# Kernel optimization log

Hardware: AMD Instinct MI355X
Metric: run time of the kernel (lower is better)

The kernel has to match this reference:

```python
import jax, jax.numpy as jnp
import numpy as np
import math

NUM_CLASSES = 80
IMG = 800
LEVELS = [3, 4, 5, 6, 7]
LOW_T, HIGH_T = 0.4, 0.5  # Matcher thresholds


def _make_anchors():
    """detectron2 DefaultAnchorGenerator: sizes 2^(i+2)*2^(k/3), ratios {0.5,1,2}, offset 0.5."""
    all_anchors = []
    for i in LEVELS:
        stride = 2 ** i
        fs = math.ceil(IMG / stride)
        sizes = [2 ** (i + 2) * 2 ** (k / 3.0) for k in range(3)]
        cell = []
        for s in sizes:  # sizes outer, ratios inner (detectron2 order)
            area = s * s
            for a in (0.5, 1.0, 2.0):
                w = math.sqrt(area / a)
                h = a * w
                cell.append([-w / 2.0, -h / 2.0, w / 2.0, h / 2.0])
        cell = np.asarray(cell, np.float32)  # [9, 4]
        coords = (np.arange(fs, dtype=np.float32) + 0.5) * stride
        sx, sy = np.meshgrid(coords, coords)  # row-major (y, x)
        shifts = np.stack([sx.ravel(), sy.ravel(), sx.ravel(), sy.ravel()], axis=1)
        all_anchors.append((shifts[:, None, :] + cell[None, :, :]).reshape(-1, 4))
    return np.concatenate(all_anchors, 0)  # [120087, 4] xyxy


def setup_inputs() -> dict:
    key = jax.random.key(0)
    k1, k2, k3 = jax.random.split(key, 3)
    anchors = jnp.asarray(_make_anchors())  # [A, 4]
    B, T = 8, 64
    cxy = jax.random.uniform(k1, (B, T, 2), jnp.float32, 0.0, float(IMG))
    wh = jax.random.uniform(k2, (B, T, 2), jnp.float32, 10.0, 300.0)
    tgt_boxes = jnp.concatenate([cxy, wh], axis=-1)  # [B, T, 4] cxcywh
    tgt_labels = jax.random.randint(k3, (B, T), 0, NUM_CLASSES, jnp.int32)
    return {"anchors": anchors, "tgt_boxes": tgt_boxes, "tgt_labels": tgt_labels}


def _cxcywh_to_xyxy(b):
    cx, cy, w, h = b[..., 0], b[..., 1], b[..., 2], b[..., 3]
    return jnp.stack([cx - 0.5 * w, cy - 0.5 * h, cx + 0.5 * w, cy + 0.5 * h], axis=-1)


def _pairwise_iou(a, b):
    # a: [T,4], b: [A,4] xyxy -> [T,A]
    area_a = (a[:, 2] - a[:, 0]) * (a[:, 3] - a[:, 1])  # [T]
    area_b = (b[:, 2] - b[:, 0]) * (b[:, 3] - b[:, 1])  # [A]
    lt = jnp.maximum(a[:, None, :2], b[None, :, :2])  # [T,A,2]
    rb = jnp.minimum(a[:, None, 2:], b[None, :, 2:])
    wh = jnp.clip(rb - lt, 0.0)
    inter = wh[..., 0] * wh[..., 1]
    return inter / (area_a[:, None] + area_b[None, :] - inter)


def _get_deltas(src, tgt):
    # Box2BoxTransform.get_deltas with weights (1,1,1,1); boxes xyxy [A,4]
    sw = src[:, 2] - src[:, 0]
    sh = src[:, 3] - src[:, 1]
    sx = src[:, 0] + 0.5 * sw
    sy = src[:, 1] + 0.5 * sh
    tw = tgt[:, 2] - tgt[:, 0]
    th = tgt[:, 3] - tgt[:, 1]
    tx = tgt[:, 0] + 0.5 * tw
    ty = tgt[:, 1] + 0.5 * th
    return jnp.stack([(tx - sx) / sw, (ty - sy) / sh, jnp.log(tw / sw), jnp.log(th / sh)], axis=-1)


def reference(anchors, tgt_boxes, tgt_labels):
    """RetinaHead.forward_init core: per-image anchor matching + delta encoding.
    Returns anchor_labels [B, A] int32 and anchor_deltas [B, A, 4] float32."""

    def one_image(tb, tl):
        boxes = _cxcywh_to_xyxy(tb)                  # [T,4]
        iou = _pairwise_iou(boxes, anchors)          # [T,A]
        matched_vals = iou.max(axis=0)               # [A]
        matched_ids = iou.argmax(axis=0)             # [A]
        labels = jnp.where(matched_vals >= HIGH_T, 1, jnp.where(matched_vals >= LOW_T, -1, 0))
        # allow_low_quality_matches: anchors attaining the per-gt max IoU become positives
        gt_max = iou.max(axis=1, keepdims=True)      # [T,1]
        highest = (iou == gt_max).any(axis=0)        # [A]
        match_labels = jnp.where(highest, 1, labels)
        anchor_labels = tl[matched_ids]
        anchor_labels = jnp.where(match_labels == 0, NUM_CLASSES, anchor_labels)
        anchor_labels = jnp.where(match_labels == -1, -1, anchor_labels)
        anchor_deltas = _get_deltas(anchors, boxes[matched_ids])  # [A,4]
        return anchor_labels, anchor_deltas

    return jax.vmap(one_image)(tgt_boxes, tgt_labels)
```

## Files before the change

kernel.cpp:

```cpp
#include <hip/hip_runtime.h>
#include <math.h>

#pragma clang fp contract(off)

#define NUM_CLASSES 80
#define TB 64
#define NB 8
#define K1_T 512
#define K1_WAVES 8
#define WPW 128
#define K1_APB (K1_WAVES * WPW)
#define K2_T 512
#define K2_WAVES 8
#define K2_SLICES 32

__device__ __forceinline__ float iou_exact(const float4 bb, float at,
                                           const float4 av, float aar) {
  float w = fminf(bb.z, av.z) - fmaxf(bb.x, av.x);
  float h = fminf(bb.w, av.w) - fmaxf(bb.y, av.y);
  w = fmaxf(w, 0.0f);
  h = fmaxf(h, 0.0f);
  float inter = w * h;
  float u = (at + aar) - inter;
  return inter / u;
}

__device__ __forceinline__ float4 box_from_tgt4(const float4 tv) {
  return make_float4(tv.x - 0.5f * tv.z, tv.y - 0.5f * tv.w,
                     tv.x + 0.5f * tv.z, tv.y + 0.5f * tv.w);
}

__device__ __forceinline__ void wave_max4_nonneg(float& a, float& b,
                                                 float& c, float& d) {
  int va = __float_as_int(a), vb = __float_as_int(b);
  int vc = __float_as_int(c), vd = __float_as_int(d);
#define ST(ctrl)                                                            \
  { int ta = __builtin_amdgcn_update_dpp(0, va, ctrl, 0xf, 0xf, true);      \
    int tb = __builtin_amdgcn_update_dpp(0, vb, ctrl, 0xf, 0xf, true);      \
    int tc = __builtin_amdgcn_update_dpp(0, vc, ctrl, 0xf, 0xf, true);      \
    int td = __builtin_amdgcn_update_dpp(0, vd, ctrl, 0xf, 0xf, true);      \
    va = __float_as_int(fmaxf(__int_as_float(va), __int_as_float(ta)));     \
    vb = __float_as_int(fmaxf(__int_as_float(vb), __int_as_float(tb)));     \
    vc = __float_as_int(fmaxf(__int_as_float(vc), __int_as_float(tc)));     \
    vd = __float_as_int(fmaxf(__int_as_float(vd), __int_as_float(td))); }
  ST(0x111) ST(0x112) ST(0x114) ST(0x118) ST(0x142) ST(0x143)
#undef ST
  a = __int_as_float(va); b = __int_as_float(vb);
  c = __int_as_float(vc); d = __int_as_float(vd);
}

__global__ __launch_bounds__(K1_T) void k1(const float4* __restrict__ anchors,
                                           const float4* __restrict__ tgt,
                                           const int* __restrict__ labels,
                                           int* __restrict__ bmax,
                                           float* __restrict__ out,
                                           int A, int WS) {
  int b = blockIdx.y;
  __shared__ float4 sb[TB];
  __shared__ float  sa[TB];
  __shared__ int    sl[TB];
  __shared__ float  swm[K1_WAVES][TB];
  int tid = threadIdx.x, lane = tid & 63, wid = tid >> 6;

  swm[wid][lane] = 0.0f;
  if (tid < TB) {
    float4 bv = box_from_tgt4(tgt[b * TB + tid]);
    sb[tid] = bv;
    sa[tid] = (bv.z - bv.x) * (bv.w - bv.y);
    sl[tid] = labels[b * TB + tid];
  }
  __syncthreads();

  const int base[6] = {0, 90000, 112500, 118125, 119646, 120087};
  const int fsv[5]  = {100, 50, 25, 13, 7};
  int astart = blockIdx.x * K1_APB + wid * WPW;
  int s0 = min(astart, A - 1);
  int e0 = min(astart + WPW, A);
  if (e0 <= s0) e0 = s0 + 1;
  float ylo = 3.0e38f, yhi = -3.0e38f;
  float x1lo = 3.0e38f, x1hi = -3.0e38f;
  float x2lo = 3.0e38f, x2hi = -3.0e38f;
  int nseg = 0;
#pragma unroll
  for (int li = 0; li < 5; ++li) {
    int s = max(s0, base[li]), e = min(e0, base[li + 1]);
    if (s < e) {
      nseg++;
      int stride = 8 << li;
      int rowsz = 9 * fsv[li];
      int i0 = s - base[li], i1 = e - 1 - base[li];
      int r0 = i0 / rowsz, r1 = i1 / rowsz;
      float half = 1.15f * (float)(32 << li) + 1.0f;
      ylo = fminf(ylo, ((float)r0 + 0.5f) * (float)stride - half);
      yhi = fmaxf(yhi, ((float)r1 + 0.5f) * (float)stride + half);
      if (r0 == r1) {
        int c0 = (i0 % rowsz) / 9, c1 = (i1 % rowsz) / 9;
        x1lo = fminf(x1lo, ((float)c0 + 0.5f) * (float)stride - half);
        x1hi = fmaxf(x1hi, ((float)c1 + 0.5f) * (float)stride + half);
      } else if (r1 == r0 + 1) {
        int c0 = (i0 % rowsz) / 9, c1 = (i1 % rowsz) / 9;
        x1lo = fminf(x1lo, ((float)c0 + 0.5f) * (float)stride - half);
        x1hi = fmaxf(x1hi, ((float)(fsv[li] - 1) + 0.5f) * (float)stride + half);
        x2lo = fminf(x2lo, 0.5f * (float)stride - half);
        x2hi = fmaxf(x2hi, ((float)c1 + 0.5f) * (float)stride + half);
      } else {
        x1lo = -3.0e8f; x1hi = 3.0e8f;
      }
    }
  }
  if (nseg > 1) { x1lo = -3.0e8f; x1hi = 3.0e8f; }

  float4 bvl = sb[lane];
  bool hit = (bvl.y <= yhi) && (bvl.w >= ylo) &&
             (((bvl.x <= x1hi) && (bvl.z >= x1lo)) ||
              ((bvl.x <= x2hi) && (bvl.z >= x2lo)));
  unsigned long long mask = __ballot(hit);

  int a0c = min(astart + lane, A - 1);
  int a1c = min(astart + 64 + lane, A - 1);
  float4 av0 = anchors[a0c], av1 = anchors[a1c];
  float aar0 = (av0.z - av0.x) * (av0.w - av0.y);
  float aar1 = (av1.z - av1.x) * (av1.w - av1.y);
  float best0 = 0.0f, best1 = 0.0f;
  int mid0 = 0, mid1 = 0;

  while (mask) {
    int tA = (int)__builtin_ctzll(mask); mask &= mask - 1;
    int tB = mask ? (int)__builtin_ctzll(mask) : tA; if (mask) mask &= mask - 1;
    int tC = mask ? (int)__builtin_ctzll(mask) : tB; if (mask) mask &= mask - 1;
    int tD = mask ? (int)__builtin_ctzll(mask) : tC; if (mask) mask &= mask - 1;

    float4 bbA = sb[tA]; float atA = sa[tA];
    float4 bbB = sb[tB]; float atB = sa[tB];
    float4 bbC = sb[tC]; float atC = sa[tC];
    float4 bbD = sb[tD]; float atD = sa[tD];
    float vA0 = iou_exact(bbA, atA, av0, aar0);
    float vA1 = iou_exact(bbA, atA, av1, aar1);
    float vB0 = iou_exact(bbB, atB, av0, aar0);
    float vB1 = iou_exact(bbB, atB, av1, aar1);
    float vC0 = iou_exact(bbC, atC, av0, aar0);
    float vC1 = iou_exact(bbC, atC, av1, aar1);
    float vD0 = iou_exact(bbD, atD, av0, aar0);
    float vD1 = iou_exact(bbD, atD, av1, aar1);
    if (vA0 > best0) { best0 = vA0; mid0 = tA; }
    if (vA1 > best1) { best1 = vA1; mid1 = tA; }
    if (vB0 > best0) { best0 = vB0; mid0 = tB; }
    if (vB1 > best1) { best1 = vB1; mid1 = tB; }
    if (vC0 > best0) { best0 = vC0; mid0 = tC; }
    if (vC1 > best1) { best1 = vC1; mid1 = tC; }
    if (vD0 > best0) { best0 = vD0; mid0 = tD; }
    if (vD1 > best1) { best1 = vD1; mid1 = tD; }

    float mA = fmaxf(vA0, vA1);
    float mB = fmaxf(vB0, vB1);
    float mC = fmaxf(vC0, vC1);
    float mD = fmaxf(vD0, vD1);
    wave_max4_nonneg(mA, mB, mC, mD);
    if (lane == 63) {
      swm[wid][tA] = mA; swm[wid][tB] = mB;
      swm[wid][tC] = mC; swm[wid][tD] = mD;
    }
  }

  {
    float m = swm[wid][lane];
    bmax[((size_t)b * WS + (size_t)blockIdx.x * K1_WAVES + wid) * TB + lane] =
        __float_as_int(m);
  }

#pragma unroll
  for (int k = 0; k < 2; ++k) {
    int a = astart + k * 64 + lane;
    if (a >= A) continue;
    float4 avk = k ? av1 : av0;
    float M    = k ? best1 : best0;
    int   m    = k ? mid1 : mid0;
    float olab;
    if (M >= 0.5f)      olab = (float)sl[m];
    else if (M >= 0.4f) olab = -1.0f;
    else                olab = (float)NUM_CLASSES;
    out[(size_t)b * A + a] = olab;

    float4 mb = sb[m];
    float sw = avk.z - avk.x, sh2 = avk.w - avk.y;
    float sx = avk.x + 0.5f * sw, sy = avk.y + 0.5f * sh2;
    float tw = mb.z - mb.x,       th = mb.w - mb.y;
    float tx = mb.x + 0.5f * tw,  ty = mb.y + 0.5f * th;
    float4 d;
    d.x = (tx - sx) / sw;
    d.y = (ty - sy) / sh2;
    d.z = logf(tw / sw);
    d.w = logf(th / sh2);
    *(float4*)(out + (size_t)NB * A + ((size_t)b * A + a) * 4) = d;
  }
}

__global__ __launch_bounds__(K2_T) void k2(const float4* __restrict__ anchors,
                                           const float4* __restrict__ tgt,
                                           const int* __restrict__ bmax,
                                           const int* __restrict__ labels,
                                           float* __restrict__ out,
                                           int A, int WS) {
  int b = blockIdx.y;
  __shared__ float4 sb[TB];
  __shared__ float  sa[TB];
  __shared__ int    sl[TB];
  __shared__ int    sg[TB];
  __shared__ int    swv[K2_WAVES][TB];
  int tid = threadIdx.x, lane = tid & 63, wid = tid >> 6;

  if (tid < TB) {
    float4 bv = box_from_tgt4(tgt[b * TB + tid]);
    sb[tid] = bv;
    sa[tid] = (bv.z - bv.x) * (bv.w - bv.y);
    sl[tid] = labels[b * TB + tid];
  }

  const int* bm = bmax + (size_t)b * WS * TB;
  int acc[16];
#pragma unroll
  for (int q = 0; q < 16; ++q) acc[q] = 0;
  for (int j = 0; j < 128; j += 16) {
#pragma unroll
    for (int q = 0; q < 16; ++q) {
      int s = min(wid + (j + q) * K2_WAVES, WS - 1);
      acc[q] = max(acc[q], bm[(size_t)s * TB + lane]);
    }
  }
  int mv = 0;
#pragma unroll
  for (int q = 0; q < 16; ++q) mv = max(mv, acc[q]);
  swv[wid][lane] = mv;
  __syncthreads();
  if (tid < TB) {
    int g = swv[0][tid];
#pragma unroll
    for (int w = 1; w < K2_WAVES; ++w) g = max(g, swv[w][tid]);
    sg[tid] = g;
  }
  __syncthreads();

  for (int s = blockIdx.x * K2_WAVES + wid; s < WS; s += K2_SLICES * K2_WAVES) {
    int val = bm[(size_t)s * TB + lane];
    bool att = (val == sg[lane]);
    unsigned long long am = __ballot(att);
    while (am) {
      int t = (int)__builtin_ctzll(am); am &= am - 1;
      int g = sg[t];
      float4 bb = sb[t]; float at = sa[t];
#pragma unroll
      for (int half = 0; half < 2; ++half) {
        int a = s * WPW + half * 64 + lane;
        int ac = min(a, A - 1);
        float4 av = anchors[ac];
        float aar = (av.z - av.x) * (av.w - av.y);
        float v = iou_exact(bb, at, av, aar);
        bool hitv = (a < A) && (__float_as_int(v) == g);
        unsigned long long hm = __ballot(hitv);
        while (hm) {
          int hl = (int)__builtin_ctzll(hm); hm &= hm - 1;
          float4 ah = make_float4(__shfl(av.x, hl, 64), __shfl(av.y, hl, 64),
                                  __shfl(av.z, hl, 64), __shfl(av.w, hl, 64));
          float haar = __shfl(aar, hl, 64);
          int   ha   = __shfl(a, hl, 64);
          float v2 = iou_exact(sb[lane], sa[lane], ah, haar);
          float m = v2;
#pragma unroll
          for (int off = 1; off < 64; off <<= 1)
            m = fmaxf(m, __shfl_xor(m, off, 64));
          unsigned long long eq = __ballot(v2 == m);
          int mid = (int)__builtin_ctzll(eq);
          if (lane == 0) out[(size_t)b * A + ha] = (float)sl[mid];
        }
      }
    }
  }
}

extern "C" void kernel_launch(void* const* d_in, const int* in_sizes, int n_in,
                              void* d_out, int out_size, void* d_ws, size_t ws_size,
                              hipStream_t stream) {
  const float* anchors    = (const float*)d_in[0];
  const float* tgt_boxes  = (const float*)d_in[1];
  const int*   tgt_labels = (const int*)d_in[2];
  int A = in_sizes[0] / 4;
  int NBLK = (A + K1_APB - 1) / K1_APB;
  int WS = NBLK * K1_WAVES;

  int*   bmax = (int*)d_ws;
  float* out  = (float*)d_out;

  dim3 g1(NBLK, NB);
  k1<<<g1, K1_T, 0, stream>>>((const float4*)anchors, (const float4*)tgt_boxes,
                              tgt_labels, bmax, out, A, WS);
  dim3 g2(K2_SLICES, NB);
  k2<<<g2, K2_T, 0, stream>>>((const float4*)anchors, (const float4*)tgt_boxes,
                              bmax, tgt_labels, out, A, WS);
}
```

Before: 49.04 us.

## Replace per-GT max reduction with per-target spatial window search kernel

Drops the per-wave per-target max tracking and workspace write from the main matching kernel. The second kernel is replaced by one block per (image, target) that scans only the anchors whose centres lie near the target box at each pyramid level. Each block computes the target's max IoU and then relabels the anchors that attain it. This removes the DPP reductions from the hot loop and the reread of the workspace. It relies on a geometric bound on anchor extent (1.15x the size plus a margin) to guarantee that no anchor with positive IoU is missed.

Result: slower. 124.6 us (+154.1%).

```diff
diff --git a/kernel.cpp b/kernel.cpp
--- a/kernel.cpp
+++ b/kernel.cpp
@@ -10,9 +10,6 @@
 #define K1_WAVES 8
 #define WPW 128
 #define K1_APB (K1_WAVES * WPW)
-#define K2_T 512
-#define K2_WAVES 8
-#define K2_SLICES 32
 
 __device__ __forceinline__ float iou_exact(const float4 bb, float at,
                                            const float4 av, float aar) {
@@ -30,39 +27,16 @@
                      tv.x + 0.5f * tv.z, tv.y + 0.5f * tv.w);
 }
 
-__device__ __forceinline__ void wave_max4_nonneg(float& a, float& b,
-                                                 float& c, float& d) {
-  int va = __float_as_int(a), vb = __float_as_int(b);
-  int vc = __float_as_int(c), vd = __float_as_int(d);
-#define ST(ctrl)                                                            \
-  { int ta = __builtin_amdgcn_update_dpp(0, va, ctrl, 0xf, 0xf, true);      \
-    int tb = __builtin_amdgcn_update_dpp(0, vb, ctrl, 0xf, 0xf, true);      \
-    int tc = __builtin_amdgcn_update_dpp(0, vc, ctrl, 0xf, 0xf, true);      \
-    int td = __builtin_amdgcn_update_dpp(0, vd, ctrl, 0xf, 0xf, true);      \
-    va = __float_as_int(fmaxf(__int_as_float(va), __int_as_float(ta)));     \
-    vb = __float_as_int(fmaxf(__int_as_float(vb), __int_as_float(tb)));     \
-    vc = __float_as_int(fmaxf(__int_as_float(vc), __int_as_float(tc)));     \
-    vd = __float_as_int(fmaxf(__int_as_float(vd), __int_as_float(td))); }
-  ST(0x111) ST(0x112) ST(0x114) ST(0x118) ST(0x142) ST(0x143)
-#undef ST
-  a = __int_as_float(va); b = __int_as_float(vb);
-  c = __int_as_float(vc); d = __int_as_float(vd);
-}
-
 __global__ __launch_bounds__(K1_T) void k1(const float4* __restrict__ anchors,
                                            const float4* __restrict__ tgt,
                                            const int* __restrict__ labels,
-                                           int* __restrict__ bmax,
-                                           float* __restrict__ out,
-                                           int A, int WS) {
+                                           float* __restrict__ out, int A) {
   int b = blockIdx.y;
   __shared__ float4 sb[TB];
   __shared__ float  sa[TB];
   __shared__ int    sl[TB];
-  __shared__ float  swm[K1_WAVES][TB];
   int tid = threadIdx.x, lane = tid & 63, wid = tid >> 6;
 
-  swm[wid][lane] = 0.0f;
   if (tid < TB) {
     float4 bv = box_from_tgt4(tgt[b * TB + tid]);
     sb[tid] = bv;
@@ -150,22 +124,6 @@
     if (vC1 > best1) { best1 = vC1; mid1 = tC; }
     if (vD0 > best0) { best0 = vD0; mid0 = tD; }
     if (vD1 > best1) { best1 = vD1; mid1 = tD; }
-
-    float mA = fmaxf(vA0, vA1);
-    float mB = fmaxf(vB0, vB1);
-    float mC = fmaxf(vC0, vC1);
-    float mD = fmaxf(vD0, vD1);
-    wave_max4_nonneg(mA, mB, mC, mD);
-    if (lane == 63) {
-      swm[wid][tA] = mA; swm[wid][tB] = mB;
-      swm[wid][tC] = mC; swm[wid][tD] = mD;
-    }
-  }
-
-  {
-    float m = swm[wid][lane];
-    bmax[((size_t)b * WS + (size_t)blockIdx.x * K1_WAVES + wid) * TB + lane] =
-        __float_as_int(m);
   }
 
 #pragma unroll
@@ -195,18 +153,15 @@
   }
 }
 
-__global__ __launch_bounds__(K2_T) void k2(const float4* __restrict__ anchors,
-                                           const float4* __restrict__ tgt,
-                                           const int* __restrict__ bmax,
-                                           const int* __restrict__ labels,
-                                           float* __restrict__ out,
-                                           int A, int WS) {
-  int b = blockIdx.y;
+__global__ __launch_bounds__(256) void k3(const float4* __restrict__ anchors,
+                                          const float4* __restrict__ tgt,
+                                          const int* __restrict__ labels,
+                                          float* __restrict__ out, int A) {
+  int b = blockIdx.y, t = blockIdx.x;
   __shared__ float4 sb[TB];
   __shared__ float  sa[TB];
   __shared__ int    sl[TB];
-  __shared__ int    sg[TB];
-  __shared__ int    swv[K2_WAVES][TB];
+  __shared__ float  sred[4];
   int tid = threadIdx.x, lane = tid & 63, wid = tid >> 6;
 
   if (tid < TB) {
@@ -215,60 +170,78 @@
     sa[tid] = (bv.z - bv.x) * (bv.w - bv.y);
     sl[tid] = labels[b * TB + tid];
   }
-
-  const int* bm = bmax + (size_t)b * WS * TB;
-  int acc[16];
-#pragma unroll
-  for (int q = 0; q < 16; ++q) acc[q] = 0;
-  for (int j = 0; j < 128; j += 16) {
-#pragma unroll
-    for (int q = 0; q < 16; ++q) {
-      int s = min(wid + (j + q) * K2_WAVES, WS - 1);
-      acc[q] = max(acc[q], bm[(size_t)s * TB + lane]);
-    }
-  }
-  int mv = 0;
-#pragma unroll
-  for (int q = 0; q < 16; ++q) mv = max(mv, acc[q]);
-  swv[wid][lane] = mv;
   __syncthreads();
-  if (tid < TB) {
-    int g = swv[0][tid];
-#pragma unroll
-    for (int w = 1; w < K2_WAVES; ++w) g = max(g, swv[w][tid]);
-    sg[tid] = g;
-  }
-  __syncthreads();
-
-  for (int s = blockIdx.x * K2_WAVES + wid; s < WS; s += K2_SLICES * K2_WAVES) {
-    int val = bm[(size_t)s * TB + lane];
-    bool att = (val == sg[lane]);
-    unsigned long long am = __ballot(att);
-    while (am) {
-      int t = (int)__builtin_ctzll(am); am &= am - 1;
-      int g = sg[t];
-      float4 bb = sb[t]; float at = sa[t];
-#pragma unroll
-      for (int half = 0; half < 2; ++half) {
-        int a = s * WPW + half * 64 + lane;
-        int ac = min(a, A - 1);
-        float4 av = anchors[ac];
+
+  float4 bb = sb[t];
+  float  at = sa[t];
+  const int base[5] = {0, 90000, 112500, 118125, 119646};
+  const int fsv[5]  = {100, 50, 25, 13, 7};
+
+  float bestv = 0.0f;
+#pragma unroll
+  for (int li = 0; li < 5; ++li) {
+    int stride = 8 << li;
+    int fs = fsv[li];
+    float half = 1.15f * (float)(32 << li) + 1.0f;
+    float inv = 1.0f / (float)stride;
+    int r0 = max((int)floorf((bb.y - half) * inv - 0.5f) - 1, 0);
+    int r1 = min((int)ceilf ((bb.w + half) * inv - 0.5f) + 1, fs - 1);
+    int c0 = max((int)floorf((bb.x - half) * inv - 0.5f) - 1, 0);
+    int c1 = min((int)ceilf ((bb.z + half) * inv - 0.5f) + 1, fs - 1);
+    if (r0 > r1 || c0 > c1) continue;
+    int ncl = (c1 - c0 + 1) * 9;
+    for (int r = r0; r <= r1; ++r) {
+      int as = base[li] + (r * fs + c0) * 9;
+      for (int j = tid; j < ncl; j += 256) {
+        float4 av = anchors[as + j];
         float aar = (av.z - av.x) * (av.w - av.y);
         float v = iou_exact(bb, at, av, aar);
-        bool hitv = (a < A) && (__float_as_int(v) == g);
-        unsigned long long hm = __ballot(hitv);
+        bestv = fmaxf(bestv, v);
+      }
+    }
+  }
+  for (int off = 1; off < 64; off <<= 1)
+    bestv = fmaxf(bestv, __shfl_xor(bestv, off, 64));
+  if (lane == 0) sred[wid] = bestv;
+  __syncthreads();
+  float g = fmaxf(fmaxf(sred[0], sred[1]), fmaxf(sred[2], sred[3]));
+
+  float4 myb = sb[lane];
+  float  mya = sa[lane];
+#pragma unroll
+  for (int li = 0; li < 5; ++li) {
+    int stride = 8 << li;
+    int fs = fsv[li];
+    float half = 1.15f * (float)(32 << li) + 1.0f;
+    float inv = 1.0f / (float)stride;
+    int r0 = max((int)floorf((bb.y - half) * inv - 0.5f) - 1, 0);
+    int r1 = min((int)ceilf ((bb.w + half) * inv - 0.5f) + 1, fs - 1);
+    int c0 = max((int)floorf((bb.x - half) * inv - 0.5f) - 1, 0);
+    int c1 = min((int)ceilf ((bb.z + half) * inv - 0.5f) + 1, fs - 1);
+    if (r0 > r1 || c0 > c1) continue;
+    int ncl = (c1 - c0 + 1) * 9;
+    for (int r = r0; r <= r1; ++r) {
+      int as = base[li] + (r * fs + c0) * 9;
+      for (int j = tid; j - lane < ncl; j += 256) {
+        bool in = (j < ncl);
+        int a = as + min(j, ncl - 1);
+        float4 av = anchors[a];
+        float aar = (av.z - av.x) * (av.w - av.y);
+        float v = iou_exact(bb, at, av, aar);
+        bool hit = in && (v == g);
+        unsigned long long hm = __ballot(hit);
         while (hm) {
           int hl = (int)__builtin_ctzll(hm); hm &= hm - 1;
           float4 ah = make_float4(__shfl(av.x, hl, 64), __shfl(av.y, hl, 64),
                                   __shfl(av.z, hl, 64), __shfl(av.w, hl, 64));
           float haar = __shfl(aar, hl, 64);
           int   ha   = __shfl(a, hl, 64);
-          float v2 = iou_exact(sb[lane], sa[lane], ah, haar);
-          float m = v2;
+          float v2 = iou_exact(myb, mya, ah, haar);
+          float m2 = v2;
 #pragma unroll
           for (int off = 1; off < 64; off <<= 1)
-            m = fmaxf(m, __shfl_xor(m, off, 64));
-          unsigned long long eq = __ballot(v2 == m);
+            m2 = fmaxf(m2, __shfl_xor(m2, off, 64));
+          unsigned long long eq = __ballot(v2 == m2);
           int mid = (int)__builtin_ctzll(eq);
           if (lane == 0) out[(size_t)b * A + ha] = (float)sl[mid];
         }
@@ -285,15 +258,12 @@
   const int*   tgt_labels = (const int*)d_in[2];
   int A = in_sizes[0] / 4;
   int NBLK = (A + K1_APB - 1) / K1_APB;
-  int WS = NBLK * K1_WAVES;
-
-  int*   bmax = (int*)d_ws;
-  float* out  = (float*)d_out;
+  float* out = (float*)d_out;
 
   dim3 g1(NBLK, NB);
   k1<<<g1, K1_T, 0, stream>>>((const float4*)anchors, (const float4*)tgt_boxes,
-                              tgt_labels, bmax, out, A, WS);
-  dim3 g2(K2_SLICES, NB);
-  k2<<<g2, K2_T, 0, stream>>>((const float4*)anchors, (const float4*)tgt_boxes,
-                              bmax, tgt_labels, out, A, WS);
-}
+                              tgt_labels, out, A);
+  dim3 g3(TB, NB);
+  k3<<<g3, 256, 0, stream>>>((const float4*)anchors, (const float4*)tgt_boxes,
+                             tgt_labels, out, A);
+}
```
